# Kernel tuning notes

Hardware: AMD Instinct MI355X
Metric: run time of the kernel (lower is better)

Reference implementation:

```python
import jax, jax.numpy as jnp
import numpy as np

DN = ('NCHW', 'OIHW', 'NCHW')

def conv3x3(x, w, b):
    y = jax.lax.conv_general_dilated(x, w, window_strides=(1, 1), padding='SAME', dimension_numbers=DN)
    return y + b[None, :, None, None]

def setup_inputs() -> dict:
    key = jax.random.key(0)
    ks = jax.random.split(key, 12)
    B, C, H, W, r = 4, 64, 128, 128, 2
    ic = C * r * r  # 256
    s = 0.02
    inp = {
        'x': jax.random.normal(ks[0], (B, C, H, W), jnp.float32),
        'g_w': jax.random.normal(ks[1], (ic, ic), jnp.float32) * s,
        'g_b': jnp.zeros((ic,), jnp.float32),
        'theta_w': jax.random.normal(ks[2], (ic, ic), jnp.float32) * s,
        'theta_b': jnp.zeros((ic,), jnp.float32),
        'phi_w': jax.random.normal(ks[3], (ic, ic), jnp.float32) * s,
        'phi_b': jnp.zeros((ic,), jnp.float32),
        'Ws_w': jax.random.normal(ks[4], (C, C), jnp.float32) * s,
        'Ws_b': jnp.zeros((C,), jnp.float32),
        'Wc_w': jax.random.normal(ks[5], (C, C), jnp.float32) * s,
        'Wc_b': jnp.zeros((C,), jnp.float32),
        'gamma_s': jnp.ones((1,), jnp.float32),
        'gamma_c': jnp.ones((1,), jnp.float32),
        'm1_w': jax.random.normal(ks[6], (16, C, 3, 3), jnp.float32) * s,
        'm1_b': jnp.zeros((16,), jnp.float32),
        'm2_w': jax.random.normal(ks[7], (1, 16, 3, 3), jnp.float32) * s,
        'm2_b': jnp.zeros((1,), jnp.float32),
    }
    return inp

def reference(x, g_w, g_b, theta_w, theta_b, phi_w, phi_b, Ws_w, Ws_b, Wc_w, Wc_b, gamma_s, gamma_c, m1_w, m1_b, m2_w, m2_b):
    b, c, h, w = x.shape
    ic = g_w.shape[0]
    r = int(round((ic // c) ** 0.5))
    hr, wr = h // r, w // r
    n = hr * wr  # spatial positions after channel-folding
    # x1: [b, ic, n] (row-major reshape, same as torch .reshape)
    x1 = x.reshape(b, ic, n)
    # 1x1 convs == channel matmuls
    g_x = jnp.einsum('oi,bin->bno', g_w, x1) + g_b          # [b, n, ic]
    th = jnp.einsum('oi,bin->bon', theta_w, x1) + theta_b[:, None]  # [b, ic, n]
    ph = jnp.einsum('oi,bin->bon', phi_w, x1) + phi_b[:, None]      # [b, ic, n]
    # spatial attention: [b, n, n]
    f_s = jnp.einsum('bcn,bcm->bnm', th, ph)
    f_s = jax.nn.softmax(f_s, axis=-1)
    y_s = jnp.einsum('bnm,bmo->bno', f_s, g_x)              # [b, n, ic]
    y_s = jnp.transpose(y_s, (0, 2, 1)).reshape(b, c, h, w)
    # channel attention: [b, ic, ic]
    f_c = jnp.einsum('bcn,bdn->bcd', th, ph)
    f_c = jax.nn.softmax(f_c, axis=-1)
    y_c = jnp.einsum('bno,bod->bnd', g_x, f_c).reshape(b, c, h, w)
    ws = jnp.einsum('oi,bihw->bohw', Ws_w, y_s) + Ws_b[None, :, None, None]
    wc = jnp.einsum('oi,bihw->bohw', Wc_w, y_c) + Wc_b[None, :, None, None]
    z = x + gamma_s[0] * ws + gamma_c[0] * wc
    hmid = jax.nn.relu(conv3x3(z, m1_w, m1_b))
    logit = conv3x3(hmid, m2_w, m2_b)
    return (logit, z)
```

## Files before the change

### kernel.cpp

```cpp
#include <hip/hip_runtime.h>
#include <stdint.h>

typedef unsigned short u16;
typedef unsigned int   u32;

typedef __attribute__((ext_vector_type(8)))  short bf16x8;
typedef __attribute__((ext_vector_type(4)))  float f32x4;

__device__ __forceinline__ float b2f(u16 u) { return __uint_as_float(((u32)u) << 16); }
__device__ __forceinline__ float blo(u32 u) { return __uint_as_float(u << 16); }
__device__ __forceinline__ float bhi(u32 u) { return __uint_as_float(u & 0xffff0000u); }
__device__ __forceinline__ u16 f2b(float f) {
    u32 x = __float_as_uint(f);
    u32 r = (x + 0x7fffu + ((x >> 16) & 1u)) >> 16;
    return (u16)r;
}

#define NB   4
#define IC   256
#define NPOS 4096
#define CH   64
#define HW   16384

__global__ __launch_bounds__(256) void prep_kernel(
    const float* __restrict__ wsw, const float* __restrict__ wcw,
    const float* __restrict__ m1w,
    const float* __restrict__ thw, const float* __restrict__ phw, const float* __restrict__ gw,
    float* __restrict__ wswT, float* __restrict__ wcwT, float* __restrict__ m1wT,
    u16* __restrict__ wbf)
{
    int idx = blockIdx.x * 256 + threadIdx.x;
    if (idx < 65536) {
        wbf[idx]          = f2b(thw[idx]);
        wbf[idx + 65536]  = f2b(phw[idx]);
        wbf[idx + 131072] = f2b(gw[idx]);
    }
    if (idx < 4096) {
        int i = idx >> 6, c = idx & 63;
        wswT[i*64 + c] = wsw[c*64 + i];
        wcwT[i*64 + c] = wcw[c*64 + i];
    }
    if (idx < 9216) {
        int o = idx & 15, ct = idx >> 4;
        int t = ct % 9, c = ct / 9;
        m1wT[idx] = m1w[(o*64 + c)*9 + t];
    }
}

__global__ __launch_bounds__(256) void qkv_mfma_kernel(
    const float* __restrict__ x, const u16* __restrict__ wbf,
    const float* __restrict__ thb, const float* __restrict__ phb, const float* __restrict__ gb,
    u16* __restrict__ Q, u16* __restrict__ K, u16* __restrict__ VT)
{
    __shared__ __align__(16) u32 xT[64*132];
    __shared__ __align__(16) float bias_l[256];
    const int tid  = threadIdx.x;
    const int w    = tid >> 6;
    const int lane = tid & 63;
    const int q4   = lane >> 4;
    const int l    = lane & 15;
    const int n0   = blockIdx.x * 64;
    const int b    = blockIdx.y;
    const int mat  = blockIdx.z;
    const u16* wmat = wbf + mat * 65536;
    const float* bias = (mat == 0) ? thb : (mat == 1) ? phb : gb;

    bias_l[tid] = bias[tid];

    {
        const float* xb = x + ((size_t)b*IC)*NPOS + n0;
        int n   = tid & 63;
        int ip0 = tid >> 6;
        #pragma unroll 4
        for (int p=0; p<32; p++){
            int ip = ip0 + p*4;
            float v0 = xb[(size_t)(2*ip  )*NPOS + n];
            float v1 = xb[(size_t)(2*ip+1)*NPOS + n];
            xT[n*132 + ip] = (u32)f2b(v0) | ((u32)f2b(v1) << 16);
        }
    }
    __syncthreads();

    f32x4 acc[4][4];
    #pragma unroll
    for (int ot=0; ot<4; ot++)
        #pragma unroll
        for (int nt=0; nt<4; nt++) acc[ot][nt] = (f32x4){0.f,0.f,0.f,0.f};

    #pragma unroll
    for (int f=0; f<8; f++){
        bf16x8 bfrag[4];
        #pragma unroll
        for (int nt=0; nt<4; nt++)
            bfrag[nt] = *(const bf16x8*)&xT[(nt*16 + l)*132 + f*16 + q4*4];
        #pragma unroll
        for (int ot=0; ot<4; ot++){
            bf16x8 afrag = *(const bf16x8*)(wmat + (size_t)(w*64 + ot*16 + l)*256 + f*32 + q4*8);
            #pragma unroll
            for (int nt=0; nt<4; nt++)
                acc[ot][nt] = __builtin_amdgcn_mfma_f32_16x16x32_bf16(afrag, bfrag[nt], acc[ot][nt], 0, 0, 0);
        }
    }
    __syncthreads();

    if (mat < 2){
        u16* zbuf = (u16*)xT;
        #pragma unroll
        for (int nt=0; nt<4; nt++)
            #pragma unroll
            for (int ot=0; ot<4; ot++){
                int o = w*64 + ot*16 + q4*4;
                float4 bv = *(const float4*)&bias_l[o];
                uint2 pk;
                pk.x = (u32)f2b(acc[ot][nt][0]+bv.x) | ((u32)f2b(acc[ot][nt][1]+bv.y) << 16);
                pk.y = (u32)f2b(acc[ot][nt][2]+bv.z) | ((u32)f2b(acc[ot][nt][3]+bv.w) << 16);
                *(uint2*)&zbuf[(nt*16 + l)*264 + o] = pk;
            }
        __syncthreads();
        u16* dst = ((mat == 0) ? Q : K) + ((size_t)(b*NPOS + n0))*IC;
        int n = tid >> 2, o0 = (tid & 3)*64;
        const u32* src = &xT[n*132 + (tid & 3)*32];
        #pragma unroll
        for (int m=0; m<8; m++)
            *(uint4*)(dst + (size_t)n*IC + o0 + m*8) = ((const uint4*)src)[m];
    } else {
        u16* zbuf = (u16*)xT;
        #pragma unroll
        for (int nt=0; nt<4; nt++)
            #pragma unroll
            for (int ot=0; ot<4; ot++){
                int o = w*64 + ot*16 + q4*4;
                int n = nt*16 + l;
                #pragma unroll
                for (int reg=0; reg<4; reg++)
                    zbuf[(o+reg)*66 + n] = f2b(acc[ot][nt][reg] + bias_l[o+reg]);
            }
        __syncthreads();
        const u32* src = &xT[tid*33];
        u32 tmp[32];
        #pragma unroll
        for (int m=0; m<32; m++) tmp[m] = src[m];
        u16* dst = VT + ((size_t)(b*IC + tid))*NPOS + n0;
        #pragma unroll
        for (int m=0; m<8; m++){
            uint4 v; v.x = tmp[m*4]; v.y = tmp[m*4+1]; v.z = tmp[m*4+2]; v.w = tmp[m*4+3];
            *(uint4*)(dst + m*8) = v;
        }
    }
}

__global__ __launch_bounds__(256) void fc_mfma_kernel(
    const u16* __restrict__ Q, const u16* __restrict__ K, float* __restrict__ fcp)
{
    __shared__ __align__(16) u16 QT[64*72];
    __shared__ __align__(16) u16 KT[64*72];
    const int tid = threadIdx.x;
    const int w   = tid >> 6;
    const int lane = tid & 63;
    const int q4  = lane >> 4;
    const int l   = lane & 15;
    const int c0  = blockIdx.x * 64;
    const int d0  = blockIdx.y * 64;
    const int b   = blockIdx.z >> 2;
    const int nseg= blockIdx.z & 3;

    f32x4 acc[4];
    #pragma unroll
    for (int dt=0; dt<4; dt++) acc[dt] = (f32x4){0.f,0.f,0.f,0.f};

    for (int chunk=0; chunk<16; chunk++){
        const int n0 = nseg*1024 + chunk*64;
        __syncthreads();
        {
            int r  = tid >> 2;
            int cq = (tid & 3) * 16;
            const u16* qs = Q + ((size_t)(b*NPOS + n0 + r))*IC + c0 + cq;
            const u16* ks = K + ((size_t)(b*NPOS + n0 + r))*IC + d0 + cq;
            u16 qv[16], kv[16];
            *(uint4*)&qv[0] = *(const uint4*)qs;
            *(uint4*)&qv[8] = *(const uint4*)(qs + 8);
            *(uint4*)&kv[0] = *(const uint4*)ks;
            *(uint4*)&kv[8] = *(const uint4*)(ks + 8);
            #pragma unroll
            for (int j=0;j<16;j++){
                QT[(cq+j)*72 + r] = qv[j];
                KT[(cq+j)*72 + r] = kv[j];
            }
        }
        __syncthreads();
        #pragma unroll
        for (int f=0; f<2; f++){
            bf16x8 af = *(const bf16x8*)&QT[(w*16 + l)*72 + f*32 + q4*8];
            #pragma unroll
            for (int dt=0; dt<4; dt++){
                bf16x8 bf2 = *(const bf16x8*)&KT[(dt*16 + l)*72 + f*32 + q4*8];
                acc[dt] = __builtin_amdgcn_mfma_f32_16x16x32_bf16(af, bf2, acc[dt], 0, 0, 0);
            }
        }
    }

    #pragma unroll
    for (int dt=0; dt<4; dt++)
        #pragma unroll
        for (int reg=0; reg<4; reg++)
            fcp[((size_t)((nseg*NB + b)*256 + c0 + w*16 + q4*4 + reg))*256 + d0 + dt*16 + l] = acc[dt][reg];
}

__global__ __launch_bounds__(256) void softmax_fc_kernel(
    const float* __restrict__ fcp, float* __restrict__ pc)
{
    __shared__ float red[8];
    const int tid = threadIdx.x;
    const int b = blockIdx.x >> 8, c = blockIdx.x & 255;
    float v = 0.f;
    #pragma unroll
    for (int s=0; s<4; s++)
        v += fcp[((size_t)((s*NB + b)*256 + c))*256 + tid];
    float m = v;
    #pragma unroll
    for (int d=32; d>=1; d>>=1) m = fmaxf(m, __shfl_xor(m, d));
    if ((tid & 63) == 0) red[tid>>6] = m;
    __syncthreads();
    m = fmaxf(fmaxf(red[0],red[1]), fmaxf(red[2],red[3]));
    float e = __expf(v - m);
    float s = e;
    #pragma unroll
    for (int d=32; d>=1; d>>=1) s += __shfl_xor(s, d);
    if ((tid & 63) == 0) red[4 + (tid>>6)] = s;
    __syncthreads();
    s = red[4]+red[5]+red[6]+red[7];
    pc[(size_t)b*65536 + (size_t)c*256 + tid] = e / s;
}

__global__ __launch_bounds__(256) void yc_kernel(
    const u16* __restrict__ VT, const float* __restrict__ pc, u16* __restrict__ ycb)
{
    __shared__ __align__(16) u16 Vt_l[32*64];
    __shared__ __align__(16) float Pt[32*64];
    const int tid = threadIdx.x;
    const int n0 = blockIdx.x * 64, d0 = blockIdx.y * 64, b = blockIdx.z;
    const int tn = tid >> 4, td = tid & 15;
    float acc[4][4];
    #pragma unroll
    for (int j=0;j<4;j++)
        #pragma unroll
        for (int d=0;d<4;d++) acc[j][d]=0.f;
    for (int ot=0; ot<8; ot++){
        int o0 = ot*32;
        __syncthreads();
        {
            int ol = tid >> 3, cc = tid & 7;
            *(uint4*)&Vt_l[ol*64 + cc*8] = *(const uint4*)(VT + ((size_t)(b*IC + o0 + ol))*NPOS + n0 + cc*8);
            const float* ps = pc + (size_t)b*65536 + (size_t)(o0 + ol)*256 + d0 + cc*8;
            *(float4*)&Pt[ol*64 + cc*8]     = *(const float4*)ps;
            *(float4*)&Pt[ol*64 + cc*8 + 4] = *(const float4*)(ps + 4);
        }
        __syncthreads();
        #pragma unroll 4
        for (int kk=0; kk<32; kk++){
            float4 pv = *(const float4*)&Pt[kk*64 + td*4];
            uint2 vp = *(const uint2*)&Vt_l[kk*64 + tn*4];
            float v0 = blo(vp.x), v1 = bhi(vp.x), v2 = blo(vp.y), v3 = bhi(vp.y);
            acc[0][0] = fmaf(v0, pv.x, acc[0][0]); acc[0][1] = fmaf(v0, pv.y, acc[0][1]);
            acc[0][2] = fmaf(v0, pv.z, acc[0][2]); acc[0][3] = fmaf(v0, pv.w, acc[0][3]);
            acc[1][0] = fmaf(v1, pv.x, acc[1][0]); acc[1][1] = fmaf(v1, pv.y, acc[1][1]);
            acc[1][2] = fmaf(v1, pv.z, acc[1][2]); acc[1][3] = fmaf(v1, pv.w, acc[1][3]);
            acc[2][0] = fmaf(v2, pv.x, acc[2][0]); acc[2][1] = fmaf(v2, pv.y, acc[2][1]);
            acc[2][2] = fmaf(v2, pv.z, acc[2][2]); acc[2][3] = fmaf(v2, pv.w, acc[2][3]);
            acc[3][0] = fmaf(v3, pv.x, acc[3][0]); acc[3][1] = fmaf(v3, pv.y, acc[3][1]);
            acc[3][2] = fmaf(v3, pv.z, acc[3][2]); acc[3][3] = fmaf(v3, pv.w, acc[3][3]);
        }
    }
    #pragma unroll
    for (int j=0;j<4;j++){
        u32 lo = (u32)f2b(acc[j][0]) | ((u32)f2b(acc[j][1]) << 16);
        u32 hi = (u32)f2b(acc[j][2]) | ((u32)f2b(acc[j][3]) << 16);
        *(uint2*)&ycb[((size_t)b*NPOS + n0 + tn*4 + j)*IC + d0 + td*4] = make_uint2(lo,hi);
    }
}

__global__ __launch_bounds__(256) void flash_mfma_kernel(
    const u16* __restrict__ Q, const u16* __restrict__ K, const u16* __restrict__ VT,
    u16* __restrict__ opart0, u16* __restrict__ opartx, float* __restrict__ lpart,
    int sshift)
{
    __shared__ __align__(16) u32 Kt[8192];
    __shared__ __align__(16) u32 Vt[8192];
    const int tid  = threadIdx.x;
    const int w    = tid >> 6;
    const int lane = tid & 63;
    const int q4   = lane >> 4;
    const int l    = lane & 15;
    const int S    = 1 << sshift;
    const int b    = blockIdx.y >> sshift;
    const int seg  = blockIdx.y & (S - 1);
    const int n0   = blockIdx.x * 64;
    const int tiles = 64 >> sshift;
    const int kt0   = seg * tiles;

    bf16x8 qf[8];
    {
        const u16* qrow = Q + ((size_t)(b*NPOS + n0 + w*16 + l))*IC;
        #pragma unroll
        for (int f=0; f<8; f++)
            qf[f] = *(const bf16x8*)(qrow + f*32 + q4*8);
    }

    f32x4 oacc[16];
    #pragma unroll
    for (int t=0;t<16;t++) oacc[t] = (f32x4){0.f,0.f,0.f,0.f};
    float lrow[4] = {0.f, 0.f, 0.f, 0.f};

    u16* Pz = (u16*)Kt + w*4096;

    for (int kti=0; kti<tiles; kti++){
        const int m0 = (kt0 + kti)*64;
        __syncthreads();
        #pragma unroll
        for (int j=0;j<8;j++){
            int call = w*8 + j;
            int r = call*2 + (lane>>5);
            int c = (lane & 31) ^ (r & 7);
            const u16* g = K + ((size_t)(b*NPOS + m0 + r))*IC + c*8;
            __builtin_amdgcn_global_load_lds(
                (const __attribute__((address_space(1))) u32*)(const void*)g,
                (__attribute__((address_space(3))) u32*)(void*)&Kt[call*256], 16, 0, 0);
        }
        #pragma unroll
        for (int j=0;j<8;j++){
            int call = w*8 + j;
            int d = call*8 + (lane>>3);
            int c = (lane & 7) ^ (d & 7);
            const u16* g = VT + ((size_t)(b*IC + d))*NPOS + m0 + c*8;
            __builtin_amdgcn_global_load_lds(
                (const __attribute__((address_space(1))) u32*)(const void*)g,
                (__attribute__((address_space(3))) u32*)(void*)&Vt[call*256], 16, 0, 0);
        }
        __syncthreads();

        f32x4 sac[4];
        #pragma unroll
        for (int t=0;t<4;t++) sac[t] = (f32x4){0.f,0.f,0.f,0.f};
        #pragma unroll
        for (int f=0; f<8; f++){
            #pragma unroll
            for (int t=0;t<4;t++){
                int r = t*16 + l;
                int c = (f*4 + q4) ^ (r & 7);
                bf16x8 kf = *(const bf16x8*)((const u16*)Kt + r*256 + c*8);
                sac[t] = __builtin_amdgcn_mfma_f32_16x16x32_bf16(qf[f], kf, sac[t], 0, 0, 0);
            }
        }
        __syncthreads();

        #pragma unroll
        for (int reg=0; reg<4; reg++){
            float p0 = __expf(sac[0][reg]), p1 = __expf(sac[1][reg]);
            float p2 = __expf(sac[2][reg]), p3 = __expf(sac[3][reg]);
            lrow[reg] += (p0+p1) + (p2+p3);
            int m = q4*4 + reg;
            Pz[m*72 + l]      = f2b(p0);
            Pz[m*72 + 16 + l] = f2b(p1);
            Pz[m*72 + 32 + l] = f2b(p2);
            Pz[m*72 + 48 + l] = f2b(p3);
        }

        #pragma unroll
        for (int s=0; s<2; s++){
            bf16x8 pa = *(const bf16x8*)(Pz + l*72 + s*32 + q4*8);
            #pragma unroll
            for (int t=0;t<16;t++){
                int d = t*16 + l;
                int c = (s*4 + q4) ^ (d & 7);
                bf16x8 vb = *(const bf16x8*)((const u16*)Vt + d*64 + c*8);
                oacc[t] = __builtin_amdgcn_mfma_f32_16x16x32_bf16(pa, vb, oacc[t], 0, 0, 0);
            }
        }
    }

    #pragma unroll
    for (int reg=0; reg<4; reg++){
        float v = lrow[reg];
        v += __shfl_xor(v, 1); v += __shfl_xor(v, 2);
        v += __shfl_xor(v, 4); v += __shfl_xor(v, 8);
        if (l == 0)
            lpart[((size_t)(seg*NB + b))*NPOS + n0 + w*16 + q4*4 + reg] = v;
    }

    __syncthreads();
    #pragma unroll
    for (int t=0;t<16;t++)
        #pragma unroll
        for (int reg=0;reg<4;reg++)
            Pz[(t*16 + l)*16 + q4*4 + reg] = f2b(oacc[t][reg]);
    u16* base = (seg == 0) ? opart0 : (opartx + (size_t)(seg-1)*((size_t)NB*IC*NPOS));
    u16* dst = base + (size_t)b*(IC*NPOS) + n0 + w*16;
    for (int p=0; p<32; p++){
        int d = p*8 + (lane>>3);
        u32 val = *(const u32*)(Pz + d*16 + (lane&7)*2);
        *(u32*)(dst + (size_t)d*NPOS + (lane&7)*2) = val;
    }
}

__global__ __launch_bounds__(256) void combine_kernel(
    u16* __restrict__ opart0, const u16* __restrict__ opartx,
    const float* __restrict__ lpart, int S)
{
    const int idx = blockIdx.x * 256 + threadIdx.x;
    const int b   = idx >> 17;
    const int rem = idx & 131071;
    const int o   = rem >> 9;
    const int n   = (rem & 511) * 8;
    const size_t base = ((size_t)b*IC + o)*NPOS + n;
    float acc[8] = {0,0,0,0,0,0,0,0};
    float L[8]   = {0,0,0,0,0,0,0,0};
    for (int s=0; s<S; s++){
        const u16* p = (s == 0) ? opart0 : (opartx + (size_t)(s-1)*((size_t)NB*IC*NPOS));
        uint4 v = *(const uint4*)(p + base);
        acc[0] += blo(v.x); acc[1] += bhi(v.x);
        acc[2] += blo(v.y); acc[3] += bhi(v.y);
        acc[4] += blo(v.z); acc[5] += bhi(v.z);
        acc[6] += blo(v.w); acc[7] += bhi(v.w);
        const float* lp = lpart + ((size_t)(s*NB + b))*NPOS + n;
        float4 l0 = *(const float4*)lp;
        float4 l1 = *(const float4*)(lp + 4);
        L[0]+=l0.x; L[1]+=l0.y; L[2]+=l0.z; L[3]+=l0.w;
        L[4]+=l1.x; L[5]+=l1.y; L[6]+=l1.z; L[7]+=l1.w;
    }
    uint4 out;
    out.x = (u32)f2b(acc[0]/L[0]) | ((u32)f2b(acc[1]/L[1]) << 16);
    out.y = (u32)f2b(acc[2]/L[2]) | ((u32)f2b(acc[3]/L[3]) << 16);
    out.z = (u32)f2b(acc[4]/L[4]) | ((u32)f2b(acc[5]/L[5]) << 16);
    out.w = (u32)f2b(acc[6]/L[6]) | ((u32)f2b(acc[7]/L[7]) << 16);
    *(uint4*)(opart0 + base) = out;
}

__global__ __launch_bounds__(256) void z_kernel(
    const float* __restrict__ x, const u16* __restrict__ ysT, const u16* __restrict__ ycb,
    const float* __restrict__ wswT, const float* __restrict__ wcwT,
    const float* __restrict__ wsb, const float* __restrict__ wcb,
    const float* __restrict__ gs, const float* __restrict__ gc,
    float* __restrict__ zout)
{
    __shared__ __align__(16) float Wsl[64*32];
    __shared__ __align__(16) float Wcl[64*32];
    const int tid = threadIdx.x;
    const int p = blockIdx.x * 256 + tid;
    const int cbase = blockIdx.y * 32;
    const int b = blockIdx.z;
    {
        int i = tid >> 2, c8 = (tid & 3) * 8;
        const float* s1 = wswT + i*64 + cbase + c8;
        const float* s2 = wcwT + i*64 + cbase + c8;
        *(float4*)&Wsl[i*32 + c8]     = *(const float4*)s1;
        *(float4*)&Wsl[i*32 + c8 + 4] = *(const float4*)(s1+4);
        *(float4*)&Wcl[i*32 + c8]     = *(const float4*)s2;
        *(float4*)&Wcl[i*32 + c8 + 4] = *(const float4*)(s2+4);
    }
    __syncthreads();
    float as[32], ac[32];
    #pragma unroll
    for (int c=0;c<32;c++){ as[c]=0.f; ac[c]=0.f; }
    const u16* ysp = ysT + (size_t)b*(IC*NPOS) + p;
    const u16* ycp = ycb + (size_t)b*(IC*NPOS) + p;
    for (int i=0;i<64;i++){
        float ysv = b2f(ysp[(size_t)i*HW]);
        float ycv = b2f(ycp[(size_t)i*HW]);
        #pragma unroll
        for (int c=0;c<32;c++){
            as[c] = fmaf(Wsl[i*32+c], ysv, as[c]);
            ac[c] = fmaf(Wcl[i*32+c], ycv, ac[c]);
        }
    }
    float gsv = gs[0], gcv = gc[0];
    #pragma unroll
    for (int c=0;c<32;c++){
        int cg = cbase + c;
        float xv = x[((size_t)b*CH + cg)*HW + p];
        float zv = fmaf(gsv, as[c] + wsb[cg], xv);
        zv = fmaf(gcv, ac[c] + wcb[cg], zv);
        zout[((size_t)b*CH + cg)*HW + p] = zv;
    }
}

__global__ __launch_bounds__(256) void conv1_kernel(
    const float* __restrict__ z, const float* __restrict__ m1wT, const float* __restrict__ m1b,
    float* __restrict__ hmid)
{
    const int tid = threadIdx.x;
    const int p = blockIdx.x * 128 + (tid & 127);
    const int oh = (tid >> 7) * 8;
    const int b = blockIdx.y;
    const int y = p >> 7, xx = p & 127;
    float acc[8];
    #pragma unroll
    for (int o=0;o<8;o++) acc[o]=0.f;
    for (int c=0;c<64;c++){
        const float* zp = z + ((size_t)b*CH + c)*HW;
        #pragma unroll
        for (int t=0;t<9;t++){
            int dy = t/3 - 1, dx = t%3 - 1;
            int yy = y + dy, xv = xx + dx;
            float zv = 0.f;
            if (yy >= 0 && yy < 128 && xv >= 0 && xv < 128) zv = zp[yy*128 + xv];
            const float* w = m1wT + (c*9 + t)*16 + oh;
            #pragma unroll
            for (int o=0;o<8;o++) acc[o] = fmaf(w[o], zv, acc[o]);
        }
    }
    #pragma unroll
    for (int o=0;o<8;o++)
        hmid[((size_t)b*16 + oh + o)*HW + p] = fmaxf(acc[o] + m1b[oh + o], 0.f);
}

__global__ __launch_bounds__(256) void conv2_kernel(
    const float* __restrict__ hmid, const float* __restrict__ m2w, const float* __restrict__ m2b,
    float* __restrict__ logit)
{
    const int idx = blockIdx.x * 256 + threadIdx.x;
    const int b = idx >> 14, p = idx & 16383;
    const int y = p >> 7, xx = p & 127;
    float acc = 0.f;
    for (int c=0;c<16;c++){
        const float* hp = hmid + ((size_t)b*16 + c)*HW;
        #pragma unroll
        for (int t=0;t<9;t++){
            int dy = t/3 - 1, dx = t%3 - 1;
            int yy = y + dy, xv = xx + dx;
            if (yy >= 0 && yy < 128 && xv >= 0 && xv < 128)
                acc = fmaf(m2w[c*9+t], hp[yy*128 + xv], acc);
        }
    }
    logit[idx] = acc + m2b[0];
}

extern "C" void kernel_launch(void* const* d_in, const int* in_sizes, int n_in,
                              void* d_out, int out_size, void* d_ws, size_t ws_size,
                              hipStream_t stream)
{
    const float* x    = (const float*)d_in[0];
    const float* g_w  = (const float*)d_in[1];
    const float* g_b  = (const float*)d_in[2];
    const float* th_w = (const float*)d_in[3];
    const float* th_b = (const float*)d_in[4];
    const float* ph_w = (const float*)d_in[5];
    const float* ph_b = (const float*)d_in[6];
    const float* ws_w = (const float*)d_in[7];
    const float* ws_b = (const float*)d_in[8];
    const float* wc_w = (const float*)d_in[9];
    const float* wc_b = (const float*)d_in[10];
    const float* gs   = (const float*)d_in[11];
    const float* gc   = (const float*)d_in[12];
    const float* m1w  = (const float*)d_in[13];
    const float* m1b  = (const float*)d_in[14];
    const float* m2w  = (const float*)d_in[15];
    const float* m2b  = (const float*)d_in[16];

    char* ws = (char*)d_ws;
    u16*   Qb   = (u16*)  (ws + 0);
    u16*   Kb   = (u16*)  (ws + 8388608);
    u16*   VTb  = (u16*)  (ws + 16777216);
    u16*   ysT  = (u16*)  (ws + 25165824);
    u16*   ycb  = (u16*)  (ws + 33554432);
    u16*   wbf  = (u16*)  (ws + 41943040);
    float* pc   = (float*)(ws + 42991616);
    float* fcp  = (float*)(ws + 44040192);
    float* hmid = (float*)(ws + 44040192);
    float* lpart= (float*)(ws + 44040192);
    float* wswT = (float*)(ws + 48234496);
    float* wcwT = (float*)(ws + 48250880);
    float* m1wT = (float*)(ws + 48267264);
    u16*   opartx = (u16*)(ws + 48304128);

    float* logit = (float*)d_out;
    float* zout  = (float*)d_out + 65536;

    int sshift = 0;
    if (ws_size >= 48304128ULL + 3ULL*8388608ULL)      sshift = 2;
    else if (ws_size >= 48304128ULL + 1ULL*8388608ULL) sshift = 1;

    prep_kernel<<<256, 256, 0, stream>>>(ws_w, wc_w, m1w, th_w, ph_w, g_w,
                                         wswT, wcwT, m1wT, wbf);
    qkv_mfma_kernel<<<dim3(64,4,3), 256, 0, stream>>>(x, wbf, th_b, ph_b, g_b, Qb, Kb, VTb);
    fc_mfma_kernel<<<dim3(4,4,16), 256, 0, stream>>>(Qb, Kb, fcp);
    softmax_fc_kernel<<<1024, 256, 0, stream>>>(fcp, pc);
    yc_kernel<<<dim3(64,4,4), 256, 0, stream>>>(VTb, pc, ycb);
    flash_mfma_kernel<<<dim3(64, NB << sshift), 256, 0, stream>>>(Qb, Kb, VTb, ysT, opartx, lpart, sshift);
    combine_kernel<<<2048, 256, 0, stream>>>(ysT, opartx, lpart, 1 << sshift);
    z_kernel<<<dim3(64,2,4), 256, 0, stream>>>(x, ysT, ycb, wswT, wcwT, ws_b, wc_b, gs, gc, zout);
    conv1_kernel<<<dim3(128,4), 256, 0, stream>>>(zout, m1wT, m1b, hmid);
    conv2_kernel<<<256, 256, 0, stream>>>(hmid, m2w, m2b, logit);
}
```

Measured before the change: 469.3 us.

## Software-pipeline K/V tile loads in flash kernel with separate P buffer

Moves the P scratch out of the K tile buffer into its own LDS array so the next K tile can be prefetched into Kt right after the QK^T MFMAs, while softmax and PV run. The next V tile is staged after PV, with partial vmcnt waits and raw s_barriers replacing full __syncthreads, and s_setprio raises priority around the MFMA sections. The goal is to hide global-to-LDS load latency behind compute. In exchange it uses more LDS (an extra 9KB), which may reduce occupancy, and it relies on hand-tuned waitcnt counts that must match the number of loads issued.

```diff
diff --git a/kernel.cpp b/kernel.cpp
--- a/kernel.cpp
+++ b/kernel.cpp
@@ -286,6 +286,7 @@
 {
     __shared__ __align__(16) u32 Kt[8192];
     __shared__ __align__(16) u32 Vt[8192];
+    __shared__ __align__(16) u16 Pl[4608];
     const int tid  = threadIdx.x;
     const int w    = tid >> 6;
     const int lane = tid & 63;
@@ -311,36 +312,48 @@
     for (int t=0;t<16;t++) oacc[t] = (f32x4){0.f,0.f,0.f,0.f};
     float lrow[4] = {0.f, 0.f, 0.f, 0.f};
 
-    u16* Pz = (u16*)Kt + w*4096;
-
-    for (int kti=0; kti<tiles; kti++){
-        const int m0 = (kt0 + kti)*64;
-        __syncthreads();
+    u16* Pz = Pl + w*1152;
+
+    auto stage_k = [&](int m0s){
         #pragma unroll
         for (int j=0;j<8;j++){
             int call = w*8 + j;
             int r = call*2 + (lane>>5);
             int c = (lane & 31) ^ (r & 7);
-            const u16* g = K + ((size_t)(b*NPOS + m0 + r))*IC + c*8;
+            const u16* g = K + ((size_t)(b*NPOS + m0s + r))*IC + c*8;
             __builtin_amdgcn_global_load_lds(
                 (const __attribute__((address_space(1))) u32*)(const void*)g,
                 (__attribute__((address_space(3))) u32*)(void*)&Kt[call*256], 16, 0, 0);
         }
+    };
+    auto stage_v = [&](int m0s){
         #pragma unroll
         for (int j=0;j<8;j++){
             int call = w*8 + j;
             int d = call*8 + (lane>>3);
             int c = (lane & 7) ^ (d & 7);
-            const u16* g = VT + ((size_t)(b*IC + d))*NPOS + m0 + c*8;
+            const u16* g = VT + ((size_t)(b*IC + d))*NPOS + m0s + c*8;
             __builtin_amdgcn_global_load_lds(
                 (const __attribute__((address_space(1))) u32*)(const void*)g,
                 (__attribute__((address_space(3))) u32*)(void*)&Vt[call*256], 16, 0, 0);
         }
-        __syncthreads();
+    };
+
+    stage_k(kt0*64);
+    stage_v(kt0*64);
+    asm volatile("s_waitcnt vmcnt(0)" ::: "memory");
+    __builtin_amdgcn_sched_barrier(0);
+    __builtin_amdgcn_s_barrier();
+    __builtin_amdgcn_sched_barrier(0);
+
+    for (int kti=0; kti<tiles; kti++){
+        const bool more = (kti + 1 < tiles);
+        const int mn = (kt0 + kti + 1)*64;
 
         f32x4 sac[4];
         #pragma unroll
         for (int t=0;t<4;t++) sac[t] = (f32x4){0.f,0.f,0.f,0.f};
+        __builtin_amdgcn_s_setprio(1);
         #pragma unroll
         for (int f=0; f<8; f++){
             #pragma unroll
@@ -351,7 +364,13 @@
                 sac[t] = __builtin_amdgcn_mfma_f32_16x16x32_bf16(qf[f], kf, sac[t], 0, 0, 0);
             }
         }
-        __syncthreads();
+        __builtin_amdgcn_s_setprio(0);
+
+        __builtin_amdgcn_sched_barrier(0);
+        __builtin_amdgcn_s_barrier();
+        __builtin_amdgcn_sched_barrier(0);
+
+        if (more) stage_k(mn);
 
         #pragma unroll
         for (int reg=0; reg<4; reg++){
@@ -365,17 +384,39 @@
             Pz[m*72 + 48 + l] = f2b(p3);
         }
 
-        #pragma unroll
-        for (int s=0; s<2; s++){
-            bf16x8 pa = *(const bf16x8*)(Pz + l*72 + s*32 + q4*8);
+        if (more) { asm volatile("s_waitcnt vmcnt(8)" ::: "memory"); }
+        else      { asm volatile("s_waitcnt vmcnt(0)" ::: "memory"); }
+        __builtin_amdgcn_sched_barrier(0);
+        __builtin_amdgcn_s_barrier();
+        __builtin_amdgcn_sched_barrier(0);
+
+        __builtin_amdgcn_s_setprio(1);
+        #pragma unroll
+        for (int s2=0; s2<2; s2++){
+            bf16x8 pa = *(const bf16x8*)(Pz + l*72 + s2*32 + q4*8);
             #pragma unroll
             for (int t=0;t<16;t++){
                 int d = t*16 + l;
-                int c = (s*4 + q4) ^ (d & 7);
+                int c = (s2*4 + q4) ^ (d & 7);
                 bf16x8 vb = *(const bf16x8*)((const u16*)Vt + d*64 + c*8);
                 oacc[t] = __builtin_amdgcn_mfma_f32_16x16x32_bf16(pa, vb, oacc[t], 0, 0, 0);
             }
         }
+        __builtin_amdgcn_s_setprio(0);
+
+        __builtin_amdgcn_sched_barrier(0);
+        __builtin_amdgcn_s_barrier();
+        __builtin_amdgcn_sched_barrier(0);
+
+        if (more) {
+            stage_v(mn);
+            asm volatile("s_waitcnt vmcnt(8)" ::: "memory");
+        } else {
+            asm volatile("s_waitcnt vmcnt(0)" ::: "memory");
+        }
+        __builtin_amdgcn_sched_barrier(0);
+        __builtin_amdgcn_s_barrier();
+        __builtin_amdgcn_sched_barrier(0);
     }
 
     #pragma unroll
@@ -388,16 +429,17 @@
     }
 
     __syncthreads();
+    u16* Ez = (u16*)Kt + w*4096;
     #pragma unroll
     for (int t=0;t<16;t++)
         #pragma unroll
         for (int reg=0;reg<4;reg++)
-            Pz[(t*16 + l)*16 + q4*4 + reg] = f2b(oacc[t][reg]);
+            Ez[(t*16 + l)*16 + q4*4 + reg] = f2b(oacc[t][reg]);
     u16* base = (seg == 0) ? opart0 : (opartx + (size_t)(seg-1)*((size_t)NB*IC*NPOS));
     u16* dst = base + (size_t)b*(IC*NPOS) + n0 + w*16;
     for (int p=0; p<32; p++){
         int d = p*8 + (lane>>3);
-        u32 val = *(const u32*)(Pz + d*16 + (lane&7)*2);
+        u32 val = *(const u32*)(Ez + d*16 + (lane&7)*2);
         *(u32*)(dst + (size_t)d*NPOS + (lane&7)*2) = val;
     }
 }
```

Result: faster. 459.4 us (-2.1%).
